# Kernel tuning notes

Hardware: AMD Instinct MI355X
Metric: run time of the kernel (lower is better)

Reference implementation:

```python
import jax, jax.numpy as jnp
import numpy as np

B, S, D_MODEL, D_HIDDEN = 4, 2048, 1024, 4096

# --- BitNet b1.58-style quantizers (STE in bwd version) ---

def act_quant(x):
    # per-token int8 absmax quantization over last dim
    scale = 127.0 / jnp.clip(jnp.max(jnp.abs(x), axis=-1, keepdims=True), 1e-5)
    return jnp.clip(jnp.round(x * scale), -128, 127) / scale

def weight_quant(w):
    # ternary weights with global mean-abs scale
    scale = 1.0 / jnp.clip(jnp.mean(jnp.abs(w)), 1e-5)
    return jnp.clip(jnp.round(w * scale), -1, 1) / scale

def bit_linear(x, w):
    # STE: forward uses quantized values, gradient passes through
    xq = x + jax.lax.stop_gradient(act_quant(x) - x)
    wq = w + jax.lax.stop_gradient(weight_quant(w) - w)
    return jnp.einsum('bsd,hd->bsh', xq, wq)

def depthwise_conv1d(x_bcl, w, b):
    # x_bcl: [B, C, L], w: [C, 1, 3], b: [C]
    y = jax.lax.conv_general_dilated(
        x_bcl, w, window_strides=(1,), padding=[(1, 1)],
        dimension_numbers=('NCH', 'OIH', 'NCH'),
        feature_group_count=x_bcl.shape[1])
    return y + b[None, :, None]


def setup_inputs() -> dict:
    key = jax.random.key(0)
    ks = jax.random.split(key, 5)
    lim1 = 1.0 / np.sqrt(D_MODEL)
    lim2 = 1.0 / np.sqrt(D_HIDDEN)
    limc = 1.0 / np.sqrt(3.0)  # fan_in = 1*3 for depthwise conv
    return {
        'x': jax.random.normal(ks[0], (B, S, D_MODEL), dtype=jnp.float32),
        'w1': jax.random.uniform(ks[1], (D_HIDDEN, D_MODEL), jnp.float32, -lim1, lim1),
        'conv_w': jax.random.uniform(ks[2], (D_HIDDEN, 1, 3), jnp.float32, -limc, limc),
        'conv_b': jax.random.uniform(ks[3], (D_HIDDEN,), jnp.float32, -limc, limc),
        'w2': jax.random.uniform(ks[4], (D_MODEL, D_HIDDEN), jnp.float32, -lim2, lim2),
    }


def reference(x, w1, conv_w, conv_b, w2):
    h = bit_linear(x, w1)                      # [B, S, H]
    h = depthwise_conv1d(h.transpose(0, 2, 1), conv_w, conv_b)  # [B, H, S]
    h = h.transpose(0, 2, 1)                   # [B, S, H]
    h = jax.nn.silu(h)
    return bit_linear(h, w2)                   # [B, S, D]
```

## Files before the change

### kernel.cpp

```cpp
#include <hip/hip_runtime.h>
#include <cstdint>

#define S_    2048
#define DM    1024
#define DH    4096
#define NTOK  8192
#define WELEM 4194304
#define CT    8

typedef int v4i __attribute__((ext_vector_type(4)));
typedef _Float16 half8 __attribute__((ext_vector_type(8)));
typedef char char8v __attribute__((ext_vector_type(8)));

#define GLOAD_LDS16(g, l)                                                   \
    __builtin_amdgcn_global_load_lds(                                       \
        (const __attribute__((address_space(1))) void*)(g),                 \
        (__attribute__((address_space(3))) void*)(l), 16, 0, 0)

static __device__ __forceinline__ void sbar() {
    asm volatile("" ::: "memory");
    __builtin_amdgcn_s_barrier();
    asm volatile("" ::: "memory");
}
#define VMC0() asm volatile("s_waitcnt vmcnt(0)" ::: "memory")
#define VMC3() asm volatile("s_waitcnt vmcnt(3)" ::: "memory")
#define VMC4() asm volatile("s_waitcnt vmcnt(4)" ::: "memory")

__global__ __launch_bounds__(256) void absmean_partial(const float4* __restrict__ wa,
                                                       const float4* __restrict__ wb,
                                                       double* __restrict__ partial) {
    __shared__ double red[256];
    const float4* w = (blockIdx.x < 1024) ? wa : wb;
    int base = (blockIdx.x & 1023) * 1024;
    double s = 0.0;
#pragma unroll
    for (int k = 0; k < 4; ++k) {
        float4 v = w[base + (k << 8) + threadIdx.x];
        s += (double)fabsf(v.x) + (double)fabsf(v.y) +
             (double)fabsf(v.z) + (double)fabsf(v.w);
    }
    red[threadIdx.x] = s;
    __syncthreads();
    for (int off = 128; off > 0; off >>= 1) {
        if (threadIdx.x < off) red[threadIdx.x] += red[threadIdx.x + off];
        __syncthreads();
    }
    if (threadIdx.x == 0) partial[blockIdx.x] = red[0];
}

__global__ __launch_bounds__(256) void finalize_scales(const double* __restrict__ part,
                                                       float* __restrict__ sc) {
    __shared__ double red[1024];
#pragma unroll 1
    for (int m = 0; m < 2; ++m) {
        const double* p = part + m * 1024;
        __syncthreads();
#pragma unroll
        for (int k = 0; k < 4; ++k) red[(k << 8) + threadIdx.x] = p[(k << 8) + threadIdx.x];
        __syncthreads();
        double s = red[threadIdx.x] + red[threadIdx.x + 256] +
                   red[threadIdx.x + 512] + red[threadIdx.x + 768];
        __syncthreads();
        red[threadIdx.x] = s;
        __syncthreads();
        for (int off = 128; off > 0; off >>= 1) {
            if (threadIdx.x < off) red[threadIdx.x] += red[threadIdx.x + off];
            __syncthreads();
        }
        if (threadIdx.x == 0) {
            double mean = red[0] / (double)WELEM;
            float mf = fmaxf((float)mean, 1e-5f);
            float scale = 1.0f / mf;
            sc[2 * m]     = scale;
            sc[2 * m + 1] = 1.0f / scale;
        }
    }
}

__global__ __launch_bounds__(256) void quant_all(const float4* __restrict__ w1,
                                                 const float4* __restrict__ w2,
                                                 const float4* __restrict__ x,
                                                 char4* __restrict__ qw1,
                                                 char4* __restrict__ qw2,
                                                 char4* __restrict__ qx,
                                                 float* __restrict__ dqx,
                                                 const float* __restrict__ sc) {
    __shared__ float red[256];
    if (blockIdx.x < 8192) {
        bool second = blockIdx.x >= 4096;
        const float4* w = second ? w2 : w1;
        char4* q = second ? qw2 : qw1;
        float scale = sc[second ? 2 : 0];
        int i = (blockIdx.x & 4095) * 256 + threadIdx.x;
        float4 v = w[i];
        char4 o;
        o.x = (signed char)(int)fminf(fmaxf(rintf(v.x * scale), -1.f), 1.f);
        o.y = (signed char)(int)fminf(fmaxf(rintf(v.y * scale), -1.f), 1.f);
        o.z = (signed char)(int)fminf(fmaxf(rintf(v.z * scale), -1.f), 1.f);
        o.w = (signed char)(int)fminf(fmaxf(rintf(v.w * scale), -1.f), 1.f);
        q[i] = o;
    } else {
        int t = blockIdx.x - 8192;
        float4 v = x[(size_t)t * 256 + threadIdx.x];
        float mx = fmaxf(fmaxf(fabsf(v.x), fabsf(v.y)), fmaxf(fabsf(v.z), fabsf(v.w)));
        red[threadIdx.x] = mx;
        __syncthreads();
        for (int off = 128; off > 0; off >>= 1) {
            if (threadIdx.x < off) red[threadIdx.x] = fmaxf(red[threadIdx.x], red[threadIdx.x + off]);
            __syncthreads();
        }
        float scale = 127.0f / fmaxf(red[0], 1e-5f);
        char4 o;
        o.x = (signed char)(int)rintf(v.x * scale);
        o.y = (signed char)(int)rintf(v.y * scale);
        o.z = (signed char)(int)rintf(v.z * scale);
        o.w = (signed char)(int)rintf(v.w * scale);
        qx[(size_t)t * 256 + threadIdx.x] = o;
        if (threadIdx.x == 0) dqx[t] = 1.0f / scale;
    }
}

__global__ __launch_bounds__(512) void conv_silu_quant(const half8* __restrict__ h,
                                                       const float4* __restrict__ cwv,
                                                       const float4* __restrict__ cbv,
                                                       char8v* __restrict__ q,
                                                       float* __restrict__ dq) {
    __shared__ float red[2][8];
    const int tid = threadIdx.x;
    const int t0 = blockIdx.x * CT;
    const int s0 = t0 & (S_ - 1);

    float wc[24], bs[8];
    {
        float4 tmp;
#pragma unroll
        for (int i = 0; i < 6; ++i) {
            tmp = cwv[tid * 6 + i];
            wc[4 * i] = tmp.x; wc[4 * i + 1] = tmp.y; wc[4 * i + 2] = tmp.z; wc[4 * i + 3] = tmp.w;
        }
        tmp = cbv[tid * 2];     bs[0] = tmp.x; bs[1] = tmp.y; bs[2] = tmp.z; bs[3] = tmp.w;
        tmp = cbv[tid * 2 + 1]; bs[4] = tmp.x; bs[5] = tmp.y; bs[6] = tmp.z; bs[7] = tmp.w;
    }

    auto ldrow = [&](int t, bool valid, float* dst) {
        if (valid) {
            half8 raw = h[(size_t)t * 512 + tid];
#pragma unroll
            for (int e = 0; e < 8; ++e) dst[e] = (float)raw[e];
        } else {
#pragma unroll
            for (int e = 0; e < 8; ++e) dst[e] = 0.f;
        }
    };

    float pv[8], cu[8], nx[8], pf[8];
    ldrow(t0 - 1, s0 > 0, pv);
    ldrow(t0, true, cu);
    ldrow(t0 + 1, true, nx);

#pragma unroll
    for (int i = 0; i < CT; ++i) {
        const int t = t0 + i;
        ldrow(t + 2, (s0 + i + 2) < S_, pf);

        float v[8];
        float mx = 0.f;
#pragma unroll
        for (int e = 0; e < 8; ++e) {
            float y = wc[3 * e] * pv[e] + wc[3 * e + 1] * cu[e] + wc[3 * e + 2] * nx[e] + bs[e];
            float ex = __builtin_amdgcn_exp2f(-1.44269504088896f * y);
            float r  = y * __builtin_amdgcn_rcpf(1.0f + ex);
            v[e] = r;
            mx = fmaxf(mx, fabsf(r));
        }
#pragma unroll
        for (int off = 32; off > 0; off >>= 1)
            mx = fmaxf(mx, __shfl_down(mx, off, 64));
        if ((tid & 63) == 0) red[i & 1][tid >> 6] = mx;
        __syncthreads();
        float rmax = red[i & 1][0];
#pragma unroll
        for (int w = 1; w < 8; ++w) rmax = fmaxf(rmax, red[i & 1][w]);
        float scale = 127.0f / fmaxf(rmax, 1e-5f);
        char8v o;
#pragma unroll
        for (int e = 0; e < 8; ++e)
            o[e] = (signed char)(int)rintf(v[e] * scale);
        q[(size_t)t * 512 + tid] = o;
        if (tid == 0) dq[t] = 1.0f / scale;
#pragma unroll
        for (int e = 0; e < 8; ++e) { pv[e] = cu[e]; cu[e] = nx[e]; nx[e] = pf[e]; }
    }
}

template <int BM, int WAVES, typename OutT>
__global__ __launch_bounds__(WAVES * 64, (BM == 256) ? 4 : 3)
void gemm_i8_bk64(const int8_t* __restrict__ A, const int8_t* __restrict__ Bm,
                  OutT* __restrict__ C, const float* __restrict__ rowdq,
                  const float* __restrict__ sc, int slot, int N, int K) {
    constexpr int BN = 128;
    constexpr int ABYTES = BM * 64;
    constexpr int BUF = (BM + BN) * 64;
    constexpr int ALOADS = BM / 16 / WAVES;
    constexpr int BLOADS = BN / 16 / WAVES;
    constexpr int L = ALOADS + BLOADS;

    __shared__ __align__(16) int8_t lds[3][BUF];
    const int tid  = threadIdx.x;
    const int lane = tid & 63;
    const int wave = tid >> 6;

    const int nwg = gridDim.x * gridDim.y;
    int flat = blockIdx.y * gridDim.x + blockIdx.x;
    flat = (flat & 7) * (nwg >> 3) + (flat >> 3);
    const int bx = flat % gridDim.x;
    const int by = flat / gridDim.x;
    const int mbase = by * BM;
    const int nbase = bx << 7;
    const int NT = K >> 6;

    const int wm = wave >> 1;
    const int wn = wave & 1;

    const int srow = lane >> 2;
    const int csrc = (((lane & 3) ^ ((lane >> 3) & 3)) << 4);
    const int8_t* Ag = A  + (size_t)(mbase + wave * (ALOADS * 16) + srow) * K + csrc;
    const int8_t* Bg = Bm + (size_t)(nbase + wave * (BLOADS * 16) + srow) * K + csrc;

    auto stage = [&](int s, int tt) {
        const size_t ko = (size_t)tt << 6;
        int8_t* dA = &lds[s][(wave * ALOADS) << 10];
        int8_t* dB = &lds[s][ABYTES + ((wave * BLOADS) << 10)];
#pragma unroll
        for (int l = 0; l < ALOADS; ++l)
            GLOAD_LDS16(Ag + ko + (size_t)(l * 16) * K, dA + (l << 10));
#pragma unroll
        for (int l = 0; l < BLOADS; ++l)
            GLOAD_LDS16(Bg + ko + (size_t)(l * 16) * K, dB + (l << 10));
    };

    const int fc   = (((lane >> 4) ^ ((lane >> 1) & 3)) << 4);
    const int aoff = ((wm * 64 + (lane & 15)) << 6) + fc;
    const int boff = ABYTES + ((wn * 64 + (lane & 15)) << 6) + fc;

    v4i acc[4][4] = {};

    stage(0, 0);
    stage(1, 1);
    if constexpr (L == 3) VMC3(); else VMC4();
    sbar();

    int sb = 0;
    for (int t = 0; t < NT; ++t) {
        const int8_t* base = &lds[sb][0];
        v4i af[4], bf[4];
#pragma unroll
        for (int i = 0; i < 4; ++i)
            af[i] = *reinterpret_cast<const v4i*>(base + aoff + (i << 10));
#pragma unroll
        for (int j = 0; j < 4; ++j)
            bf[j] = *reinterpret_cast<const v4i*>(base + boff + (j << 10));
        int s2 = sb + 2; if (s2 >= 3) s2 -= 3;
        if (t + 2 < NT) stage(s2, t + 2);

        __builtin_amdgcn_s_setprio(1);
#pragma unroll
        for (int i = 0; i < 4; ++i)
#pragma unroll
            for (int j = 0; j < 4; ++j)
                acc[i][j] = __builtin_amdgcn_mfma_i32_16x16x64_i8(af[i], bf[j], acc[i][j], 0, 0, 0);
        __builtin_amdgcn_s_setprio(0);

        if (t + 2 < NT)      { if constexpr (L == 3) VMC3(); else VMC4(); }
        else if (t + 1 < NT) VMC0();
        sbar();
        if (++sb == 3) sb = 0;
    }

    const float wdq = sc[slot];
    const int quad = lane >> 4;
    const int col  = lane & 15;
#pragma unroll
    for (int i = 0; i < 4; ++i) {
#pragma unroll
        for (int r = 0; r < 4; ++r) {
            int m = mbase + (wm << 6) + (i << 4) + (quad << 2) + r;
            float rs = rowdq[m] * wdq;
#pragma unroll
            for (int j = 0; j < 4; ++j) {
                int n = nbase + (wn << 6) + (j << 4) + col;
                C[(size_t)m * N + n] = (OutT)((float)acc[i][j][r] * rs);
            }
        }
    }
}

extern "C" void kernel_launch(void* const* d_in, const int* in_sizes, int n_in,
                              void* d_out, int out_size, void* d_ws, size_t ws_size,
                              hipStream_t stream) {
    const float* x  = (const float*)d_in[0];
    const float* w1 = (const float*)d_in[1];
    const float* cw = (const float*)d_in[2];
    const float* cb = (const float*)d_in[3];
    const float* w2 = (const float*)d_in[4];
    float* out = (float*)d_out;
    char* ws = (char*)d_ws;

    double* part  = (double*)(ws + 0);
    float*  sc    = (float*)(ws + 16384);
    float*  dqx   = (float*)(ws + 16640);
    float*  dqh   = (float*)(ws + 49408);
    int8_t* qw1   = (int8_t*)(ws + 82176);
    int8_t* qw2   = (int8_t*)(ws + 4276480);
    int8_t* qx    = (int8_t*)(ws + 8470784);
    int8_t* qh    = (int8_t*)(ws + 16859392);
    _Float16* h   = (_Float16*)(ws + 50413824);

    absmean_partial<<<2048, 256, 0, stream>>>((const float4*)w1, (const float4*)w2, part);
    finalize_scales<<<1, 256, 0, stream>>>(part, sc);
    quant_all<<<16384, 256, 0, stream>>>((const float4*)w1, (const float4*)w2,
                                         (const float4*)x, (char4*)qw1, (char4*)qw2,
                                         (char4*)qx, dqx, sc);

    dim3 g1(DH / 128, NTOK / 256);
    gemm_i8_bk64<256, 8, _Float16><<<g1, 512, 0, stream>>>(qx, qw1, h, dqx, sc, 1, DH, DM);

    conv_silu_quant<<<NTOK / CT, 512, 0, stream>>>((const half8*)h, (const float4*)cw,
                                                   (const float4*)cb, (char8v*)qh, dqh);

    dim3 g2(DM / 128, NTOK / 128);
    gemm_i8_bk64<128, 4, float><<<g2, 256, 0, stream>>>(qh, qw2, out, dqh, sc, 3, DM, DH);
}
```

Measured before the change: 232.4 us.

## Use 256x256 tile int8 GEMM with double-buffered LDS for first layer

After: 495.5 us. 2.13x slower.

```diff
diff --git a/kernel.cpp b/kernel.cpp
--- a/kernel.cpp
+++ b/kernel.cpp
@@ -193,6 +193,113 @@
     }
 }
 
+template <typename OutT>
+__global__ __launch_bounds__(512, 4)
+void gemm_i8_w128(const int8_t* __restrict__ A, const int8_t* __restrict__ Bm,
+                  OutT* __restrict__ C, const float* __restrict__ rowdq,
+                  const float* __restrict__ sc, int slot, int N, int K) {
+    __shared__ __align__(16) int8_t lds[2][32768];
+    const int tid  = threadIdx.x;
+    const int lane = tid & 63;
+    const int wave = tid >> 6;
+
+    const int nwg = gridDim.x * gridDim.y;
+    int flat = blockIdx.y * gridDim.x + blockIdx.x;
+    flat = (flat & 7) * (nwg >> 3) + (flat >> 3);
+    const int bx = flat % gridDim.x;
+    const int by = flat / gridDim.x;
+    const int mbase = by << 8;
+    const int nbase = bx << 8;
+    const int NT = K >> 6;
+
+    const int wm = wave >> 2;
+    const int wn = wave & 3;
+
+    const int srow = lane >> 2;
+    const int csrc = (((lane & 3) ^ ((lane >> 3) & 3)) << 4);
+    const int8_t* Ag = A  + (size_t)(mbase + wave * 32 + srow) * K + csrc;
+    const int8_t* Bg = Bm + (size_t)(nbase + wave * 32 + srow) * K + csrc;
+
+    auto stageA = [&](int s, int tt) {
+        const size_t ko = (size_t)tt << 6;
+        int8_t* d = &lds[s][wave << 11];
+        GLOAD_LDS16(Ag + ko,                  d);
+        GLOAD_LDS16(Ag + ko + (size_t)16 * K, d + 1024);
+    };
+    auto stageB = [&](int s, int tt) {
+        const size_t ko = (size_t)tt << 6;
+        int8_t* d = &lds[s][16384 + (wave << 11)];
+        GLOAD_LDS16(Bg + ko,                  d);
+        GLOAD_LDS16(Bg + ko + (size_t)16 * K, d + 1024);
+    };
+
+    const int fc   = (((lane >> 4) ^ ((lane >> 1) & 3)) << 4);
+    const int aoff = ((wm * 128 + (lane & 15)) << 6) + fc;
+    const int boff = 16384 + ((wn * 64 + (lane & 15)) << 6) + fc;
+
+    v4i acc[8][4] = {};
+
+    stageA(0, 0); stageB(0, 0);
+    VMC0();
+    sbar();
+
+    for (int t = 0; t < NT; ++t) {
+        const int8_t* base = &lds[t & 1][0];
+        const int nb = (t & 1) ^ 1;
+
+        v4i bf[4], af0[4];
+#pragma unroll
+        for (int j = 0; j < 4; ++j)
+            bf[j] = *reinterpret_cast<const v4i*>(base + boff + (j << 10));
+#pragma unroll
+        for (int i = 0; i < 4; ++i)
+            af0[i] = *reinterpret_cast<const v4i*>(base + aoff + (i << 10));
+        if (t + 1 < NT) stageA(nb, t + 1);
+
+        __builtin_amdgcn_s_setprio(1);
+#pragma unroll
+        for (int i = 0; i < 4; ++i)
+#pragma unroll
+            for (int j = 0; j < 4; ++j)
+                acc[i][j] = __builtin_amdgcn_mfma_i32_16x16x64_i8(af0[i], bf[j], acc[i][j], 0, 0, 0);
+        __builtin_amdgcn_s_setprio(0);
+
+        v4i af1[4];
+#pragma unroll
+        for (int i = 0; i < 4; ++i)
+            af1[i] = *reinterpret_cast<const v4i*>(base + aoff + ((i + 4) << 10));
+        if (t + 1 < NT) stageB(nb, t + 1);
+
+        __builtin_amdgcn_s_setprio(1);
+#pragma unroll
+        for (int i = 0; i < 4; ++i)
+#pragma unroll
+            for (int j = 0; j < 4; ++j)
+                acc[i + 4][j] = __builtin_amdgcn_mfma_i32_16x16x64_i8(af1[i], bf[j], acc[i + 4][j], 0, 0, 0);
+        __builtin_amdgcn_s_setprio(0);
+
+        if (t + 1 < NT) VMC0();
+        sbar();
+    }
+
+    const float wdq = sc[slot];
+    const int quad = lane >> 4;
+    const int col  = lane & 15;
+#pragma unroll
+    for (int i = 0; i < 8; ++i) {
+#pragma unroll
+        for (int r = 0; r < 4; ++r) {
+            int m = mbase + (wm << 7) + (i << 4) + (quad << 2) + r;
+            float rs = rowdq[m] * wdq;
+#pragma unroll
+            for (int j = 0; j < 4; ++j) {
+                int n = nbase + (wn << 6) + (j << 4) + col;
+                C[(size_t)m * N + n] = (OutT)((float)acc[i][j][r] * rs);
+            }
+        }
+    }
+}
+
 template <int BM, int WAVES, typename OutT>
 __global__ __launch_bounds__(WAVES * 64, (BM == 256) ? 4 : 3)
 void gemm_i8_bk64(const int8_t* __restrict__ A, const int8_t* __restrict__ Bm,
@@ -322,8 +429,8 @@
                                          (const float4*)x, (char4*)qw1, (char4*)qw2,
                                          (char4*)qx, dqx, sc);
 
-    dim3 g1(DH / 128, NTOK / 256);
-    gemm_i8_bk64<256, 8, _Float16><<<g1, 512, 0, stream>>>(qx, qw1, h, dqx, sc, 1, DH, DM);
+    dim3 g1(DH / 256, NTOK / 256);
+    gemm_i8_w128<_Float16><<<g1, 512, 0, stream>>>(qx, qw1, h, dqx, sc, 1, DH, DM);
 
     conv_silu_quant<<<NTOK / CT, 512, 0, stream>>>((const half8*)h, (const float4*)cw,
                                                    (const float4*)cb, (char8v*)qh, dqh);
```
